# Performance work log

Measured on AMD Instinct MI355X. Metric: run time of the kernel, lower is better.

## Reference

```python
import jax, jax.numpy as jnp
import numpy as np

B, C, H, W = 8, 384, 32, 32
NUM_HEADS = 8
HEAD_DIM = C // NUM_HEADS
HIDDEN = max(32, C // 2)


def setup_inputs() -> dict:
    key = jax.random.key(0)
    ks = jax.random.split(key, 6)
    s = lambda fan_in: 1.0 / np.sqrt(fan_in)
    return {
        "x": jax.random.normal(ks[0], (B, C, H, W), dtype=jnp.float32),
        "qkv_w": jax.random.normal(ks[1], (C, 3 * C), dtype=jnp.float32) * s(C),
        "qkv_b": jnp.zeros((3 * C,), dtype=jnp.float32),
        "proj_w": jax.random.normal(ks[2], (C, C), dtype=jnp.float32) * s(C),
        "proj_b": jnp.zeros((C,), dtype=jnp.float32),
        "mlp_w1": jax.random.normal(ks[3], (2, HIDDEN), dtype=jnp.float32) * s(2),
        "mlp_b1": jnp.zeros((HIDDEN,), dtype=jnp.float32),
        "mlp_w2": jax.random.normal(ks[4], (HIDDEN, NUM_HEADS), dtype=jnp.float32) * s(HIDDEN),
        "mlp_b2": jnp.zeros((NUM_HEADS,), dtype=jnp.float32),
    }


def _relative_bias(h, w, mlp_w1, mlp_b1, mlp_w2, mlp_b2):
    ch = jnp.arange(h, dtype=jnp.float32)
    cw = jnp.arange(w, dtype=jnp.float32)
    coords = jnp.stack(jnp.meshgrid(ch, cw, indexing="ij"), axis=-1).reshape(-1, 2)  # [N,2]
    rel = coords[:, None, :] - coords[None, :, :]  # [N,N,2]
    denom = jnp.array([max(h - 1, 1), max(w - 1, 1)], dtype=jnp.float32)
    rel = rel / denom
    hidden = jax.nn.gelu(rel @ mlp_w1 + mlp_b1, approximate=False)
    bias = hidden @ mlp_w2 + mlp_b2  # [N,N,heads]
    return jnp.transpose(bias, (2, 0, 1))  # [heads,N,N]


def reference(x, qkv_w, qkv_b, proj_w, proj_b, mlp_w1, mlp_b1, mlp_w2, mlp_b2):
    b, c, h, w = x.shape
    n = h * w
    tokens = x.reshape(b, c, n).transpose(0, 2, 1)  # [B,N,C]
    qkv = (tokens @ qkv_w + qkv_b).reshape(b, n, 3, NUM_HEADS, HEAD_DIM)
    qkv = jnp.transpose(qkv, (2, 0, 3, 1, 4))  # [3,B,h,N,d]
    q, k, v = qkv[0], qkv[1], qkv[2]
    scale = HEAD_DIM ** -0.5
    attn = jnp.einsum("bhnd,bhmd->bhnm", q * scale, k)
    attn = attn + _relative_bias(h, w, mlp_w1, mlp_b1, mlp_w2, mlp_b2)[None]
    attn = jax.nn.softmax(attn, axis=-1)
    out = jnp.einsum("bhnm,bhmd->bhnd", attn, v)
    out = out.transpose(0, 2, 1, 3).reshape(b, n, c)
    out = out @ proj_w + proj_b
    return out.transpose(0, 2, 1).reshape(b, c, h, w)
```

## Files before the change

### kernel.cpp

```cpp
#include <hip/hip_runtime.h>
#include <hip/hip_bf16.h>
#include <math.h>

#define BB 8
#define CC 384
#define NT 1024
#define NHEAD 8
#define HD 48
#define HIDDEN 192
#define THREEC 1152

typedef short short8 __attribute__((ext_vector_type(8)));
typedef short short4v __attribute__((ext_vector_type(4)));
typedef float f32x4 __attribute__((ext_vector_type(4)));
typedef unsigned int uint2v __attribute__((ext_vector_type(2)));

static __device__ __forceinline__ short bf16bits(float v) {
  __hip_bfloat16 h = __float2bfloat16(v);
  return *(short*)&h;
}
static __device__ __forceinline__ unsigned pk2(float a, float b) {
  return __builtin_amdgcn_perm(__float_as_uint(b) + 0x8000u,
                               __float_as_uint(a) + 0x8000u, 0x07060302u);
}
static __device__ __forceinline__ void lds_dma16(const void* g, void* l) {
  __builtin_amdgcn_global_load_lds((const __attribute__((address_space(1))) unsigned*)g,
                                   (__attribute__((address_space(3))) unsigned*)l, 16, 0, 0);
}

__global__ __launch_bounds__(256) void k_prep(
    const float* __restrict__ x, const float* __restrict__ qkv_w,
    const float* __restrict__ proj_w,
    const float* __restrict__ w1, const float* __restrict__ b1,
    const float* __restrict__ w2, const float* __restrict__ b2,
    __hip_bfloat16* __restrict__ xt, __hip_bfloat16* __restrict__ wtq,
    __hip_bfloat16* __restrict__ wtp, float* __restrict__ tab) {
  const int bid = blockIdx.x;
  const int tid = threadIdx.x;
  if (bid >= 3648) {
    int g = (bid - 3648) * 256 + tid;
    int p = g >> 3, jc = g & 7;
    if (p >= 63 * 63) return;
    float rh = (float)(p / 63 - 31) * (1.0f / 31.0f);
    float rw = (float)(p % 63 - 31) * (1.0f / 31.0f);
    float acc[8] = {0.f, 0.f, 0.f, 0.f, 0.f, 0.f, 0.f, 0.f};
    const int j0 = jc * 24;
#pragma unroll 4
    for (int j = j0; j < j0 + 24; j++) {
      float pre = fmaf(rh, w1[j], fmaf(rw, w1[HIDDEN + j], b1[j]));
      float gl = 0.5f * pre * (1.0f + erff(pre * 0.70710678118654752f));
#pragma unroll
      for (int h = 0; h < 8; h++) acc[h] = fmaf(gl, w2[j * 8 + h], acc[h]);
    }
#pragma unroll
    for (int msk = 1; msk <= 4; msk <<= 1)
#pragma unroll
      for (int h = 0; h < 8; h++) acc[h] += __shfl_xor(acc[h], msk);
    if (jc == 0) {
#pragma unroll
      for (int h = 0; h < 8; h++)
        tab[h * 3969 + p] = (acc[h] + b2[h]) * 1.4426950408889634f;
    }
    return;
  }
  const float* src;
  __hip_bfloat16* dst;
  int R, C, r0, c0;
  if (bid < 3072) {
    int zi = bid / 384, rem = bid % 384;
    R = 384; C = 1024;
    r0 = (rem / 32) * 32; c0 = (rem % 32) * 32;
    src = x + (size_t)zi * R * C;
    dst = xt + (size_t)zi * R * C;
  } else if (bid < 3504) {
    int i = bid - 3072;
    R = 384; C = 1152;
    r0 = (i / 36) * 32; c0 = (i % 36) * 32;
    src = qkv_w; dst = wtq;
  } else {
    int i = bid - 3504;
    R = 384; C = 384;
    r0 = (i / 12) * 32; c0 = (i % 12) * 32;
    src = proj_w; dst = wtp;
  }
  __shared__ float t[32][33];
#pragma unroll
  for (int e = 0; e < 4; e++) {
    int i = tid + e * 256;
    int r = i >> 5, c = i & 31;
    t[r][c] = src[(size_t)(r0 + r) * C + c0 + c];
  }
  __syncthreads();
#pragma unroll
  for (int e = 0; e < 4; e++) {
    int i = tid + e * 256;
    int c = i >> 5, r = i & 31;
    dst[(size_t)(c0 + c) * R + r0 + r] = __float2bfloat16(t[r][c]);
  }
}

__global__ __launch_bounds__(256) void k_qkv_mfma(
    const __hip_bfloat16* __restrict__ xt,
    const __hip_bfloat16* __restrict__ wtq,
    const float* __restrict__ qkv_b,
    __hip_bfloat16* __restrict__ Qb,
    __hip_bfloat16* __restrict__ Kb,
    __hip_bfloat16* __restrict__ Vt)
{
  __shared__ __align__(16) char smem[17408];
  short* As = (short*)smem;
  short* Bs = (short*)(smem + 8192);
  float* Vf = (float*)smem;
  const int n0 = blockIdx.x * 64;
  const int m0 = blockIdx.y * 64;
  const int tid = threadIdx.x;
  const int wv = tid >> 6, lane = tid & 63, quad = lane >> 4, lq = lane & 15;
  const int lrow = lane >> 3;
  const int gsw = ((lane & 7) ^ lrow) * 8;
  const int sw0 = (quad ^ (lq & 7)) * 8;
  const int sw1 = sw0 ^ 32;
  f32x4 acc[4];
#pragma unroll
  for (int nt = 0; nt < 4; nt++) acc[nt] = (f32x4){0.f, 0.f, 0.f, 0.f};
  for (int kk = 0; kk < CC; kk += 64) {
    __syncthreads();
    for (int c = wv; c < 16; c += 4) {
      if (c < 8)
        lds_dma16((const short*)xt + (size_t)(m0 + c * 8 + lrow) * 384 + kk + gsw,
                  smem + c * 1024);
      else
        lds_dma16((const short*)wtq + (size_t)(n0 + (c - 8) * 8 + lrow) * 384 + kk + gsw,
                  smem + 8192 + (c - 8) * 1024);
    }
    __syncthreads();
    short8 a0 = *(const short8*)(As + (wv * 16 + lq) * 64 + sw0);
    short8 a1 = *(const short8*)(As + (wv * 16 + lq) * 64 + sw1);
#pragma unroll
    for (int nt = 0; nt < 4; nt++) {
      acc[nt] = __builtin_amdgcn_mfma_f32_16x16x32_bf16(
          a0, *(const short8*)(Bs + (nt * 16 + lq) * 64 + sw0), acc[nt], 0, 0, 0);
      acc[nt] = __builtin_amdgcn_mfma_f32_16x16x32_bf16(
          a1, *(const short8*)(Bs + (nt * 16 + lq) * 64 + sw1), acc[nt], 0, 0, 0);
    }
  }
  __syncthreads();
  const float qscale = 0.14433756729740643f * 1.4426950408889634f;
  const float sc = (n0 < 384) ? qscale : 1.0f;
#pragma unroll
  for (int nt = 0; nt < 4; nt++) {
    float bias = qkv_b[n0 + nt * 16 + lq];
#pragma unroll
    for (int r = 0; r < 4; r++)
      Vf[(nt * 16 + lq) * 68 + wv * 16 + quad * 4 + r] = (acc[nt][r] + bias) * sc;
  }
  __syncthreads();
  if (n0 >= 768) {
    int ch = tid & 63, grp = tid >> 6;
    int cg = n0 - 768 + ch;
    int head = cg / 48, d = cg - head * 48;
    int b = m0 >> 10;
    int n = (m0 & 1023) + grp * 16;
    const float* src = Vf + ch * 68 + grp * 16;
    short o16[16];
#pragma unroll
    for (int k = 0; k < 16; k++) o16[k] = bf16bits(src[k]);
    short* dst = (short*)Vt + ((size_t)(b * 8 + head) * 48 + d) * 1024 + n;
    *(short8*)dst = *(short8*)o16;
    *(short8*)(dst + 8) = *(short8*)(o16 + 8);
  } else {
    const int which = n0 >= 384;
    short* Out = which ? (short*)Kb : (short*)Qb;
    int n_l = tid & 63, seg = tid >> 6;
    int rr0 = (n0 - which * 384) + seg * 16;
    int head = rr0 / 48, d0 = rr0 - head * 48;
    int b = m0 >> 10;
    int n_g = (m0 & 1023) + n_l;
    const float* src = Vf + (seg * 16) * 68 + n_l;
    short o16[16];
#pragma unroll
    for (int k = 0; k < 16; k++) o16[k] = bf16bits(src[k * 68]);
    short* dst = Out + (((size_t)(b * 8 + head) << 10) + n_g) * 64 + d0;
    *(short8*)dst = *(short8*)o16;
    *(short8*)(dst + 8) = *(short8*)(o16 + 8);
    if (d0 == 0) {
      short8 z = (short8){0, 0, 0, 0, 0, 0, 0, 0};
      *(short8*)(dst + 48) = z;
      *(short8*)(dst + 56) = z;
    }
  }
}

#define K0_OFF 0
#define K1_OFF 8192
#define V0_OFF 16384
#define V1_OFF 22528
#define TR_OFF 28672
#define PS_OFF 30720
#define SMEM_SZ 39936
__global__ __launch_bounds__(256, 4) void k_flash(
    const __hip_bfloat16* __restrict__ Qb, const __hip_bfloat16* __restrict__ Kb,
    const __hip_bfloat16* __restrict__ Vt, const float* __restrict__ tab,
    __hip_bfloat16* __restrict__ ATb)
{
  __shared__ __align__(16) char smem[SMEM_SZ];
  short* Ps_l = (short*)(smem + PS_OFF);
  float* Os = (float*)smem;

  const int tid = threadIdx.x;
  const int wv = tid >> 6, lane = tid & 63, quad = lane >> 4, lq = lane & 15;
  const int bh = blockIdx.x;
  const int q0 = blockIdx.y * 64;
  const int b = bh >> 3, h = bh & 7;
  const int inr0 = q0 >> 5;

  const int nrow = q0 + wv * 16 + lq;
  const int jnr = nrow & 31;
  const int rloc = (nrow >> 5) - inr0 + 1;
  const int tbase = rloc * 63 + jnr + 31 - 4 * quad;

  short8 qf0, qf1;
  {
    const short* qp = (const short*)Qb + ((size_t)(bh << 10) + nrow) * 64;
    qf0 = *(const short8*)(qp + quad * 8);
    qf1 = *(const short8*)(qp + 32 + quad * 8);
  }
  short8 onesv;
#pragma unroll
  for (int j = 0; j < 8; j++) onesv[j] = (short)0x3F80;

  f32x4 O[4];
#pragma unroll
  for (int dt = 0; dt < 4; dt++) O[dt] = (f32x4){0.f, 0.f, 0.f, 0.f};

  const short* kgp = (const short*)Kb + ((size_t)(bh << 10)) * 64;
  const short* vgp = (const short*)Vt + (size_t)bh * 48 * 1024;
  const float* tabg = tab + h * 3969;
  const int lrow = lane >> 3;
  const int gsw = ((lane & 7) ^ lrow) * 8;
  const int sw0 = (quad ^ (lq & 7)) * 8;
  const int sw1 = sw0 ^ 32;

  for (int c = wv; c < 15; c += 4) {
    if (c < 8)
      lds_dma16(kgp + (size_t)(c * 8 + lrow) * 64 + gsw, smem + K0_OFF + c * 1024);
    else if (c < 14)
      lds_dma16(vgp + (size_t)((c - 8) * 8 + lrow) * 1024 + gsw,
                smem + V0_OFF + (c - 8) * 1024);
    else
      lds_dma16(tabg + (inr0 + 30) * 63 + lane * 4, smem + TR_OFF);
  }

  for (int it = 0; it < 16; it++) {
    const int m0 = it * 64;
    const int buf = it & 1;
    __syncthreads();
    if (it < 15) {
      const int nbuf = buf ^ 1;
      const int mn = m0 + 64;
      for (int c = wv; c < 15; c += 4) {
        if (c < 8)
          lds_dma16(kgp + (size_t)(mn + c * 8 + lrow) * 64 + gsw,
                    smem + K0_OFF + nbuf * 8192 + c * 1024);
        else if (c < 14)
          lds_dma16(vgp + (size_t)((c - 8) * 8 + lrow) * 1024 + mn + gsw,
                    smem + V0_OFF + nbuf * 6144 + (c - 8) * 1024);
        else
          lds_dma16(tabg + (inr0 + 28 - 2 * it) * 63 + lane * 4,
                    smem + TR_OFF + nbuf * 1024);
      }
    }
    const short* Kl = (const short*)(smem + K0_OFF + buf * 8192);
    const short* Vl = (const short*)(smem + V0_OFF + buf * 6144);
    const float* Tl = (const float*)(smem + TR_OFF + buf * 1024);

    float s[4][4];
#pragma unroll
    for (int nt = 0; nt < 4; nt++) {
      const float* tn = Tl + tbase - (nt >= 2 ? 63 : 0) - (nt & 1) * 16;
      f32x4 c;
      c[0] = tn[0]; c[1] = tn[-1]; c[2] = tn[-2]; c[3] = tn[-3];
      c = __builtin_amdgcn_mfma_f32_16x16x32_bf16(
          *(const short8*)(Kl + (nt * 16 + lq) * 64 + sw0), qf0, c, 0, 0, 0);
      c = __builtin_amdgcn_mfma_f32_16x16x32_bf16(
          *(const short8*)(Kl + (nt * 16 + lq) * 64 + sw1), qf1, c, 0, 0, 0);
#pragma unroll
      for (int r = 0; r < 4; r++) s[nt][r] = c[r];
    }
#pragma unroll
    for (int nt = 0; nt < 4; nt++)
#pragma unroll
      for (int r = 0; r < 4; r++) s[nt][r] = exp2f(s[nt][r]);
#pragma unroll
    for (int nt = 0; nt < 4; nt++) {
      uint2v pw;
      pw[0] = pk2(s[nt][0], s[nt][1]);
      pw[1] = pk2(s[nt][2], s[nt][3]);
      *(uint2v*)(Ps_l + (wv * 16 + lq) * 72 + nt * 16 + quad * 4) = pw;
    }
#pragma unroll
    for (int ks = 0; ks < 2; ks++) {
      short8 pf = *(const short8*)(Ps_l + (wv * 16 + lq) * 72 + ks * 32 + quad * 8);
      const int sws = ks ? sw1 : sw0;
#pragma unroll
      for (int dt = 0; dt < 3; dt++)
        O[dt] = __builtin_amdgcn_mfma_f32_16x16x32_bf16(
            *(const short8*)(Vl + (dt * 16 + lq) * 64 + sws), pf, O[dt], 0, 0, 0);
      O[3] = __builtin_amdgcn_mfma_f32_16x16x32_bf16(onesv, pf, O[3], 0, 0, 0);
    }
  }
  float inv = 1.0f / O[3][0];
  __syncthreads();
#pragma unroll
  for (int dt = 0; dt < 3; dt++)
#pragma unroll
    for (int r = 0; r < 4; r++)
      Os[(wv * 16 + lq) * 52 + dt * 16 + quad * 4 + r] = O[dt][r] * inv;
  __syncthreads();
  {
    int row = tid >> 2, cg = (tid & 3) * 12;
    const float* src = Os + row * 52 + cg;
    short outp[12];
#pragma unroll
    for (int k = 0; k < 12; k++) outp[k] = bf16bits(src[k]);
    short* dst = (short*)ATb + ((size_t)(b << 10) + q0 + row) * 384 + h * 48 + cg;
    *(short4v*)dst = *(short4v*)outp;
    *(short4v*)(dst + 4) = *(short4v*)(outp + 4);
    *(short4v*)(dst + 8) = *(short4v*)(outp + 8);
  }
}

__global__ __launch_bounds__(256) void k_proj_mfma(
    const __hip_bfloat16* __restrict__ ATb,
    const __hip_bfloat16* __restrict__ wtp,
    const float* __restrict__ pb, float* __restrict__ out) {
  __shared__ __align__(16) char smem[16384];
  short* As = (short*)smem;
  short* Bs = (short*)(smem + 8192);
  const int c0 = blockIdx.x * 64;
  const int n0 = blockIdx.y * 64;
  const int b = blockIdx.z;
  const int tid = threadIdx.x;
  const int wv = tid >> 6, lane = tid & 63, quad = lane >> 4, lq = lane & 15;
  const int lrow = lane >> 3;
  const int gsw = ((lane & 7) ^ lrow) * 8;
  const int sw0 = (quad ^ (lq & 7)) * 8;
  const int sw1 = sw0 ^ 32;
  f32x4 acc[4];
#pragma unroll
  for (int nt = 0; nt < 4; nt++) acc[nt] = (f32x4){0.f, 0.f, 0.f, 0.f};
  for (int kk = 0; kk < CC; kk += 64) {
    __syncthreads();
    for (int c = wv; c < 16; c += 4) {
      if (c < 8)
        lds_dma16((const short*)wtp + (size_t)(c0 + c * 8 + lrow) * 384 + kk + gsw,
                  smem + c * 1024);
      else
        lds_dma16((const short*)ATb + ((size_t)(b << 10) + n0 + (c - 8) * 8 + lrow) * 384 + kk + gsw,
                  smem + 8192 + (c - 8) * 1024);
    }
    __syncthreads();
    short8 a0 = *(const short8*)(As + (wv * 16 + lq) * 64 + sw0);
    short8 a1 = *(const short8*)(As + (wv * 16 + lq) * 64 + sw1);
#pragma unroll
    for (int nt = 0; nt < 4; nt++) {
      acc[nt] = __builtin_amdgcn_mfma_f32_16x16x32_bf16(
          a0, *(const short8*)(Bs + (nt * 16 + lq) * 64 + sw0), acc[nt], 0, 0, 0);
      acc[nt] = __builtin_amdgcn_mfma_f32_16x16x32_bf16(
          a1, *(const short8*)(Bs + (nt * 16 + lq) * 64 + sw1), acc[nt], 0, 0, 0);
    }
  }
#pragma unroll
  for (int nt = 0; nt < 4; nt++) {
    int n = n0 + nt * 16 + lq;
#pragma unroll
    for (int r = 0; r < 4; r++) {
      int c = c0 + wv * 16 + quad * 4 + r;
      out[((size_t)b * 384 + c) * 1024 + n] = acc[nt][r] + pb[c];
    }
  }
}

extern "C" void kernel_launch(void* const* d_in, const int* in_sizes, int n_in,
                              void* d_out, int out_size, void* d_ws, size_t ws_size,
                              hipStream_t stream) {
  const float* x = (const float*)d_in[0];
  const float* qkv_w = (const float*)d_in[1];
  const float* qkv_b = (const float*)d_in[2];
  const float* proj_w = (const float*)d_in[3];
  const float* proj_b = (const float*)d_in[4];
  const float* w1 = (const float*)d_in[5];
  const float* b1 = (const float*)d_in[6];
  const float* w2 = (const float*)d_in[7];
  const float* b2 = (const float*)d_in[8];
  float* out = (float*)d_out;

  char* w = (char*)d_ws;
  __hip_bfloat16* xt = (__hip_bfloat16*)w;   w += (size_t)8192 * 384 * 2;
  __hip_bfloat16* wtq = (__hip_bfloat16*)w;  w += (size_t)1152 * 384 * 2;
  __hip_bfloat16* wtp = (__hip_bfloat16*)w;  w += (size_t)384 * 384 * 2;
  __hip_bfloat16* Qb = (__hip_bfloat16*)w;   w += (size_t)64 * 1024 * 64 * 2;
  __hip_bfloat16* Kb = (__hip_bfloat16*)w;   w += (size_t)64 * 1024 * 64 * 2;
  __hip_bfloat16* Vt = (__hip_bfloat16*)w;   w += (size_t)64 * 48 * 1024 * 2;
  __hip_bfloat16* ATb = (__hip_bfloat16*)w;  w += (size_t)8192 * 384 * 2;
  float* tab = (float*)w;                    w += (size_t)8 * 3969 * 4 + 1024;

  k_prep<<<dim3(3773), dim3(256), 0, stream>>>(x, qkv_w, proj_w, w1, b1, w2, b2,
                                               xt, wtq, wtp, tab);
  k_qkv_mfma<<<dim3(18, 128), dim3(256), 0, stream>>>(xt, wtq, qkv_b, Qb, Kb, Vt);
  k_flash<<<dim3(64, 16), dim3(256), 0, stream>>>(Qb, Kb, Vt, tab, ATb);
  k_proj_mfma<<<dim3(6, 16, 8), dim3(256), 0, stream>>>(ATb, wtp, proj_b, out);
}
```

Before: 164.0 us.

## Enlarge QKV and projection GEMM tiles to 128x128 with 4x4 per-warp MFMA blocking

The QKV and output-projection GEMMs move from 64x64 to 128x128 block tiles, with each wave computing a 64x64 sub-tile as a 4x4 grid of MFMAs. This raises register-level operand reuse and halves the global-to-LDS traffic per FLOP. The QKV epilogue is rewritten into a two-pass LDS staging scheme with packed 16-byte bf16 stores. Explicit waitcnt drains are added before barriers, including in the flash kernel, for correctness of the async LDS DMA. The trade-off is far fewer blocks (576 and 192), which may underfill the GPU, plus higher register and LDS usage.

```diff
diff --git a/kernel.cpp b/kernel.cpp
--- a/kernel.cpp
+++ b/kernel.cpp
@@ -14,6 +14,7 @@
 typedef short short4v __attribute__((ext_vector_type(4)));
 typedef float f32x4 __attribute__((ext_vector_type(4)));
 typedef unsigned int uint2v __attribute__((ext_vector_type(2)));
+typedef unsigned int uint4v __attribute__((ext_vector_type(4)));
 
 static __device__ __forceinline__ short bf16bits(float v) {
   __hip_bfloat16 h = __float2bfloat16(v);
@@ -27,6 +28,7 @@
   __builtin_amdgcn_global_load_lds((const __attribute__((address_space(1))) unsigned*)g,
                                    (__attribute__((address_space(3))) unsigned*)l, 16, 0, 0);
 }
+static __device__ __forceinline__ void drain_all() { __builtin_amdgcn_s_waitcnt(0); }
 
 __global__ __launch_bounds__(256) void k_prep(
     const float* __restrict__ x, const float* __restrict__ qkv_w,
@@ -107,85 +109,123 @@
     __hip_bfloat16* __restrict__ Kb,
     __hip_bfloat16* __restrict__ Vt)
 {
-  __shared__ __align__(16) char smem[17408];
+  __shared__ __align__(16) char smem[34816];
   short* As = (short*)smem;
-  short* Bs = (short*)(smem + 8192);
+  short* Bs = (short*)(smem + 16384);
   float* Vf = (float*)smem;
-  const int n0 = blockIdx.x * 64;
-  const int m0 = blockIdx.y * 64;
+  const int n0 = blockIdx.x * 128;
+  const int m0 = blockIdx.y * 128;
   const int tid = threadIdx.x;
   const int wv = tid >> 6, lane = tid & 63, quad = lane >> 4, lq = lane & 15;
+  const int msub = (wv >> 1) * 64, nsub = (wv & 1) * 64;
   const int lrow = lane >> 3;
   const int gsw = ((lane & 7) ^ lrow) * 8;
   const int sw0 = (quad ^ (lq & 7)) * 8;
   const int sw1 = sw0 ^ 32;
-  f32x4 acc[4];
-#pragma unroll
-  for (int nt = 0; nt < 4; nt++) acc[nt] = (f32x4){0.f, 0.f, 0.f, 0.f};
+  f32x4 acc[4][4];
+#pragma unroll
+  for (int mt = 0; mt < 4; mt++)
+#pragma unroll
+    for (int nt = 0; nt < 4; nt++) acc[mt][nt] = (f32x4){0.f, 0.f, 0.f, 0.f};
   for (int kk = 0; kk < CC; kk += 64) {
-    __syncthreads();
-    for (int c = wv; c < 16; c += 4) {
-      if (c < 8)
+    drain_all();
+    __syncthreads();
+    for (int c = wv; c < 32; c += 4) {
+      if (c < 16)
         lds_dma16((const short*)xt + (size_t)(m0 + c * 8 + lrow) * 384 + kk + gsw,
                   smem + c * 1024);
       else
-        lds_dma16((const short*)wtq + (size_t)(n0 + (c - 8) * 8 + lrow) * 384 + kk + gsw,
-                  smem + 8192 + (c - 8) * 1024);
-    }
-    __syncthreads();
-    short8 a0 = *(const short8*)(As + (wv * 16 + lq) * 64 + sw0);
-    short8 a1 = *(const short8*)(As + (wv * 16 + lq) * 64 + sw1);
-#pragma unroll
-    for (int nt = 0; nt < 4; nt++) {
-      acc[nt] = __builtin_amdgcn_mfma_f32_16x16x32_bf16(
-          a0, *(const short8*)(Bs + (nt * 16 + lq) * 64 + sw0), acc[nt], 0, 0, 0);
-      acc[nt] = __builtin_amdgcn_mfma_f32_16x16x32_bf16(
-          a1, *(const short8*)(Bs + (nt * 16 + lq) * 64 + sw1), acc[nt], 0, 0, 0);
-    }
-  }
-  __syncthreads();
+        lds_dma16((const short*)wtq + (size_t)(n0 + (c - 16) * 8 + lrow) * 384 + kk + gsw,
+                  smem + 16384 + (c - 16) * 1024);
+    }
+    drain_all();
+    __syncthreads();
+#pragma unroll
+    for (int ks = 0; ks < 2; ks++) {
+      const int sws = ks ? sw1 : sw0;
+      short8 af[4], bf[4];
+#pragma unroll
+      for (int t = 0; t < 4; t++) {
+        af[t] = *(const short8*)(As + (msub + t * 16 + lq) * 64 + sws);
+        bf[t] = *(const short8*)(Bs + (nsub + t * 16 + lq) * 64 + sws);
+      }
+#pragma unroll
+      for (int mt = 0; mt < 4; mt++)
+#pragma unroll
+        for (int nt = 0; nt < 4; nt++)
+          acc[mt][nt] = __builtin_amdgcn_mfma_f32_16x16x32_bf16(af[mt], bf[nt], acc[mt][nt], 0, 0, 0);
+    }
+  }
   const float qscale = 0.14433756729740643f * 1.4426950408889634f;
   const float sc = (n0 < 384) ? qscale : 1.0f;
-#pragma unroll
-  for (int nt = 0; nt < 4; nt++) {
-    float bias = qkv_b[n0 + nt * 16 + lq];
-#pragma unroll
-    for (int r = 0; r < 4; r++)
-      Vf[(nt * 16 + lq) * 68 + wv * 16 + quad * 4 + r] = (acc[nt][r] + bias) * sc;
-  }
-  __syncthreads();
-  if (n0 >= 768) {
-    int ch = tid & 63, grp = tid >> 6;
-    int cg = n0 - 768 + ch;
-    int head = cg / 48, d = cg - head * 48;
-    int b = m0 >> 10;
-    int n = (m0 & 1023) + grp * 16;
-    const float* src = Vf + ch * 68 + grp * 16;
-    short o16[16];
-#pragma unroll
-    for (int k = 0; k < 16; k++) o16[k] = bf16bits(src[k]);
-    short* dst = (short*)Vt + ((size_t)(b * 8 + head) * 48 + d) * 1024 + n;
-    *(short8*)dst = *(short8*)o16;
-    *(short8*)(dst + 8) = *(short8*)(o16 + 8);
-  } else {
-    const int which = n0 >= 384;
-    short* Out = which ? (short*)Kb : (short*)Qb;
-    int n_l = tid & 63, seg = tid >> 6;
-    int rr0 = (n0 - which * 384) + seg * 16;
-    int head = rr0 / 48, d0 = rr0 - head * 48;
-    int b = m0 >> 10;
-    int n_g = (m0 & 1023) + n_l;
-    const float* src = Vf + (seg * 16) * 68 + n_l;
-    short o16[16];
-#pragma unroll
-    for (int k = 0; k < 16; k++) o16[k] = bf16bits(src[k * 68]);
-    short* dst = Out + (((size_t)(b * 8 + head) << 10) + n_g) * 64 + d0;
-    *(short8*)dst = *(short8*)o16;
-    *(short8*)(dst + 8) = *(short8*)(o16 + 8);
-    if (d0 == 0) {
-      short8 z = (short8){0, 0, 0, 0, 0, 0, 0, 0};
-      *(short8*)(dst + 48) = z;
-      *(short8*)(dst + 56) = z;
+  const int bb = m0 >> 10;
+  const int isV = n0 >= 768;
+#pragma unroll
+  for (int p = 0; p < 2; p++) {
+    drain_all();
+    __syncthreads();
+    if ((wv & 1) == p) {
+      if (isV) {
+#pragma unroll
+        for (int nt = 0; nt < 4; nt++) {
+          float bias = qkv_b[n0 + p * 64 + nt * 16 + lq];
+#pragma unroll
+          for (int mt = 0; mt < 4; mt++)
+#pragma unroll
+            for (int r = 0; r < 4; r++)
+              Vf[(nt * 16 + lq) * 132 + msub + mt * 16 + quad * 4 + r] = acc[mt][nt][r] + bias;
+        }
+      } else {
+#pragma unroll
+        for (int nt = 0; nt < 4; nt++) {
+          float bias = qkv_b[n0 + p * 64 + nt * 16 + lq];
+#pragma unroll
+          for (int mt = 0; mt < 4; mt++)
+#pragma unroll
+            for (int r = 0; r < 4; r++)
+              Vf[(msub + mt * 16 + quad * 4 + r) * 68 + nt * 16 + lq] =
+                  (acc[mt][nt][r] + bias) * sc;
+        }
+      }
+    }
+    drain_all();
+    __syncthreads();
+    if (isV) {
+#pragma unroll
+      for (int e = 0; e < 4; e++) {
+        int i = tid + e * 256;
+        int ch = i >> 4, tk = (i & 15) * 8;
+        int cg = n0 - 768 + p * 64 + ch;
+        int head = cg / 48, d = cg - head * 48;
+        const float* s8 = Vf + ch * 132 + tk;
+        f32x4 a = *(const f32x4*)s8, b2 = *(const f32x4*)(s8 + 4);
+        uint4v o;
+        o[0] = pk2(a[0], a[1]); o[1] = pk2(a[2], a[3]);
+        o[2] = pk2(b2[0], b2[1]); o[3] = pk2(b2[2], b2[3]);
+        *(uint4v*)((short*)Vt + ((size_t)(bb * 8 + head) * 48 + d) * 1024 + (m0 & 1023) + tk) = o;
+      }
+    } else {
+      const int which = n0 >= 384;
+      short* Out = which ? (short*)Kb : (short*)Qb;
+#pragma unroll
+      for (int e = 0; e < 4; e++) {
+        int i = tid + e * 256;
+        int token = i >> 3, c8 = (i & 7) * 8;
+        int cg = (n0 - which * 384) + p * 64 + c8;
+        int head = cg / 48, d0 = cg - head * 48;
+        const float* s8 = Vf + token * 68 + c8;
+        f32x4 a = *(const f32x4*)s8, b2 = *(const f32x4*)(s8 + 4);
+        uint4v o;
+        o[0] = pk2(a[0], a[1]); o[1] = pk2(a[2], a[3]);
+        o[2] = pk2(b2[0], b2[1]); o[3] = pk2(b2[2], b2[3]);
+        short* dst = Out + (((size_t)(bb * 8 + head) << 10) + (m0 & 1023) + token) * 64 + d0;
+        *(uint4v*)dst = o;
+        if (d0 == 40) {
+          uint4v z = (uint4v){0u, 0u, 0u, 0u};
+          *(uint4v*)(dst + 8) = z;
+          *(uint4v*)(dst + 16) = z;
+        }
+      }
     }
   }
 }
@@ -253,6 +293,7 @@
   for (int it = 0; it < 16; it++) {
     const int m0 = it * 64;
     const int buf = it & 1;
+    drain_all();
     __syncthreads();
     if (it < 15) {
       const int nbuf = buf ^ 1;
@@ -309,12 +350,14 @@
     }
   }
   float inv = 1.0f / O[3][0];
+  drain_all();
   __syncthreads();
 #pragma unroll
   for (int dt = 0; dt < 3; dt++)
 #pragma unroll
     for (int r = 0; r < 4; r++)
       Os[(wv * 16 + lq) * 52 + dt * 16 + quad * 4 + r] = O[dt][r] * inv;
+  drain_all();
   __syncthreads();
   {
     int row = tid >> 2, cg = (tid & 3) * 12;
@@ -333,51 +376,63 @@
     const __hip_bfloat16* __restrict__ ATb,
     const __hip_bfloat16* __restrict__ wtp,
     const float* __restrict__ pb, float* __restrict__ out) {
-  __shared__ __align__(16) char smem[16384];
+  __shared__ __align__(16) char smem[32768];
   short* As = (short*)smem;
-  short* Bs = (short*)(smem + 8192);
-  const int c0 = blockIdx.x * 64;
-  const int n0 = blockIdx.y * 64;
+  short* Bs = (short*)(smem + 16384);
+  const int c0 = blockIdx.x * 128;
+  const int n0 = blockIdx.y * 128;
   const int b = blockIdx.z;
   const int tid = threadIdx.x;
   const int wv = tid >> 6, lane = tid & 63, quad = lane >> 4, lq = lane & 15;
+  const int msub = (wv >> 1) * 64, nsub = (wv & 1) * 64;
   const int lrow = lane >> 3;
   const int gsw = ((lane & 7) ^ lrow) * 8;
   const int sw0 = (quad ^ (lq & 7)) * 8;
   const int sw1 = sw0 ^ 32;
-  f32x4 acc[4];
-#pragma unroll
-  for (int nt = 0; nt < 4; nt++) acc[nt] = (f32x4){0.f, 0.f, 0.f, 0.f};
+  f32x4 acc[4][4];
+#pragma unroll
+  for (int mt = 0; mt < 4; mt++)
+#pragma unroll
+    for (int nt = 0; nt < 4; nt++) acc[mt][nt] = (f32x4){0.f, 0.f, 0.f, 0.f};
   for (int kk = 0; kk < CC; kk += 64) {
-    __syncthreads();
-    for (int c = wv; c < 16; c += 4) {
-      if (c < 8)
+    drain_all();
+    __syncthreads();
+    for (int c = wv; c < 32; c += 4) {
+      if (c < 16)
         lds_dma16((const short*)wtp + (size_t)(c0 + c * 8 + lrow) * 384 + kk + gsw,
                   smem + c * 1024);
       else
-        lds_dma16((const short*)ATb + ((size_t)(b << 10) + n0 + (c - 8) * 8 + lrow) * 384 + kk + gsw,
-                  smem + 8192 + (c - 8) * 1024);
-    }
-    __syncthreads();
-    short8 a0 = *(const short8*)(As + (wv * 16 + lq) * 64 + sw0);
-    short8 a1 = *(const short8*)(As + (wv * 16 + lq) * 64 + sw1);
-#pragma unroll
-    for (int nt = 0; nt < 4; nt++) {
-      acc[nt] = __builtin_amdgcn_mfma_f32_16x16x32_bf16(
-          a0, *(const short8*)(Bs + (nt * 16 + lq) * 64 + sw0), acc[nt], 0, 0, 0);
-      acc[nt] = __builtin_amdgcn_mfma_f32_16x16x32_bf16(
-          a1, *(const short8*)(Bs + (nt * 16 + lq) * 64 + sw1), acc[nt], 0, 0, 0);
-    }
-  }
-#pragma unroll
-  for (int nt = 0; nt < 4; nt++) {
-    int n = n0 + nt * 16 + lq;
+        lds_dma16((const short*)ATb + ((size_t)(b << 10) + n0 + (c - 16) * 8 + lrow) * 384 + kk + gsw,
+                  smem + 16384 + (c - 16) * 1024);
+    }
+    drain_all();
+    __syncthreads();
+#pragma unroll
+    for (int ks = 0; ks < 2; ks++) {
+      const int sws = ks ? sw1 : sw0;
+      short8 af[4], bf[4];
+#pragma unroll
+      for (int t = 0; t < 4; t++) {
+        af[t] = *(const short8*)(As + (msub + t * 16 + lq) * 64 + sws);
+        bf[t] = *(const short8*)(Bs + (nsub + t * 16 + lq) * 64 + sws);
+      }
+#pragma unroll
+      for (int mt = 0; mt < 4; mt++)
+#pragma unroll
+        for (int nt = 0; nt < 4; nt++)
+          acc[mt][nt] = __builtin_amdgcn_mfma_f32_16x16x32_bf16(af[mt], bf[nt], acc[mt][nt], 0, 0, 0);
+    }
+  }
+#pragma unroll
+  for (int mt = 0; mt < 4; mt++)
 #pragma unroll
     for (int r = 0; r < 4; r++) {
-      int c = c0 + wv * 16 + quad * 4 + r;
-      out[((size_t)b * 384 + c) * 1024 + n] = acc[nt][r] + pb[c];
-    }
-  }
+      int c = c0 + msub + mt * 16 + quad * 4 + r;
+      float bc = pb[c];
+      float* dst = out + ((size_t)b * 384 + c) * 1024 + n0 + nsub;
+#pragma unroll
+      for (int nt = 0; nt < 4; nt++) dst[nt * 16 + lq] = acc[mt][nt][r] + bc;
+    }
 }
 
 extern "C" void kernel_launch(void* const* d_in, const int* in_sizes, int n_in,
@@ -402,11 +457,11 @@
   __hip_bfloat16* Kb = (__hip_bfloat16*)w;   w += (size_t)64 * 1024 * 64 * 2;
   __hip_bfloat16* Vt = (__hip_bfloat16*)w;   w += (size_t)64 * 48 * 1024 * 2;
   __hip_bfloat16* ATb = (__hip_bfloat16*)w;  w += (size_t)8192 * 384 * 2;
-  float* tab = (float*)w;                    w += (size_t)8 * 3969 * 4 + 1024;
+  float* tab = (float*)w;                    w += (size_t)8 * 3969 * 4 + 2048;
 
   k_prep<<<dim3(3773), dim3(256), 0, stream>>>(x, qkv_w, proj_w, w1, b1, w2, b2,
                                                xt, wtq, wtp, tab);
-  k_qkv_mfma<<<dim3(18, 128), dim3(256), 0, stream>>>(xt, wtq, qkv_b, Qb, Kb, Vt);
+  k_qkv_mfma<<<dim3(9, 64), dim3(256), 0, stream>>>(xt, wtq, qkv_b, Qb, Kb, Vt);
   k_flash<<<dim3(64, 16), dim3(256), 0, stream>>>(Qb, Kb, Vt, tab, ATb);
-  k_proj_mfma<<<dim3(6, 16, 8), dim3(256), 0, stream>>>(ATb, wtp, proj_b, out);
-}
+  k_proj_mfma<<<dim3(3, 8, 8), dim3(256), 0, stream>>>(ATb, wtp, proj_b, out);
+}
```

After: 184.2 us. 1.12x slower.
